# Performance work log

Measured on AMD Instinct MI355X. Metric: run time of the kernel, lower is better.

Reference implementation:

```python
import jax, jax.numpy as jnp
import numpy as np

B, S, D = 2, 2048, 1024
H = 16
HD = D // H
SCALE = float(np.sqrt(HD))


def setup_inputs() -> dict:
    key = jax.random.key(0)
    ks = jax.random.split(key, 10)
    def lin(k):
        # xavier_uniform for [out, in] = [D, D]
        bound = float(np.sqrt(6.0 / (D + D)))
        return jax.random.uniform(k, (D, D), jnp.float32, -bound, bound)
    return {
        "hidden_states": jax.random.normal(ks[0], (B, S, D), jnp.float32),
        "attention_mask": jnp.ones((B, S), jnp.float32),
        "Wq": lin(ks[1]), "bq": jnp.zeros((D,), jnp.float32),
        "Wk": lin(ks[2]), "bk": jnp.zeros((D,), jnp.float32),
        "Wv": lin(ks[3]), "bv": jnp.zeros((D,), jnp.float32),
        "Wo": lin(ks[4]), "bo": jnp.zeros((D,), jnp.float32),
    }


def _heads(x):
    # [B,S,D] -> [B,H,S,HD]
    return x.reshape(B, S, H, HD).transpose(0, 2, 1, 3)


def secure_softmax(scores):
    c = jnp.clip(scores, -3.0, 3.0)
    sig = 0.5 + 0.25 * c - 0.01 * c ** 3
    sig = jnp.clip(sig, 0.01, 0.99)
    return sig / (jnp.sum(sig, axis=-1, keepdims=True) + 1e-8)


def reference(hidden_states, attention_mask, Wq, bq, Wk, bk, Wv, bv, Wo, bo):
    q = _heads(hidden_states @ Wq.T + bq)
    k = _heads(hidden_states @ Wk.T + bk)
    v = _heads(hidden_states @ Wv.T + bv)
    # [B,H,S,S]
    scores = jnp.einsum("bhqd,bhkd->bhqk", q, k) / SCALE
    scores = scores + (1.0 - attention_mask[:, None, None, :]) * -10000.0
    probs = secure_softmax(scores)
    ctx = jnp.einsum("bhqk,bhkd->bhqd", probs, v)
    ctx = ctx.transpose(0, 2, 1, 3).reshape(B, S, D)
    return ctx @ Wo.T + bo
```

## Files before the change

### kernel.cpp

```cpp
#include <hip/hip_runtime.h>
#include <stdint.h>

#define B_ 2
#define S_ 2048
#define D_ 1024
#define H_ 16
#define HD_ 64
#define M_ (B_*S_)

typedef __bf16 bf16;
typedef __attribute__((ext_vector_type(8))) __bf16 bf16x8;
typedef __attribute__((ext_vector_type(4))) float f32x4;
typedef __attribute__((ext_vector_type(2))) float f32x2;

__device__ __forceinline__ void gload16(const bf16* g, bf16* l) {
    __builtin_amdgcn_global_load_lds(
        (const __attribute__((address_space(1))) void*)g,
        (__attribute__((address_space(3))) void*)l, 16, 0, 0);
}

__global__ void k_cvt_all(const float* __restrict__ hs,
                          const float* __restrict__ Wq, const float* __restrict__ Wk,
                          const float* __restrict__ Wv, const float* __restrict__ Wo,
                          bf16* __restrict__ hb,
                          bf16* __restrict__ wqb, bf16* __restrict__ wkb,
                          bf16* __restrict__ wvb, bf16* __restrict__ wob) {
    int blk = blockIdx.x;
    const float* s; bf16* d; int base;
    if (blk < 2048) { s = hs; d = hb; base = blk; }
    else {
        int r = blk - 2048; int which = r >> 9; base = r & 511;
        s = (which==0)?Wq:(which==1)?Wk:(which==2)?Wv:Wo;
        d = (which==0)?wqb:(which==1)?wkb:(which==2)?wvb:wob;
    }
    int idx = base*2048 + threadIdx.x*8;
    float4 a = *(const float4*)(s + idx);
    float4 b = *(const float4*)(s + idx + 4);
    bf16 o[8] = {(bf16)a.x,(bf16)a.y,(bf16)a.z,(bf16)a.w,
                 (bf16)b.x,(bf16)b.y,(bf16)b.z,(bf16)b.w};
    *(int4*)(d + idx) = *(const int4*)o;
}

__global__ __launch_bounds__(256) void k_gemm_qkv(
    const bf16* __restrict__ X,
    const bf16* __restrict__ Wq, const bf16* __restrict__ Wk, const bf16* __restrict__ Wv,
    const float* __restrict__ bq, const float* __restrict__ bk, const float* __restrict__ bv,
    bf16* __restrict__ Qo, bf16* __restrict__ Ko, bf16* __restrict__ Vo)
{
    const int z = blockIdx.z;
    const bf16* W = (z==0) ? Wq : (z==1) ? Wk : Wv;
    const float* bias = (z==0) ? bq : (z==1) ? bk : bv;
    const int n0 = blockIdx.x * 128;
    const int m0 = blockIdx.y * 128;
    const int t = threadIdx.x;
    const int w = t >> 6, lane = t & 63, quad = lane >> 4, l15 = lane & 15;
    const int lr = lane >> 3;
    const int lc = (lane & 7) ^ lr;
    const int sx = l15 & 7;
    const int mw = (w >> 1) * 64, nw = (w & 1) * 64;

    __shared__ __align__(16) char smraw[128*136*2];
    bf16* As  = (bf16*)smraw;
    bf16* Bs  = (bf16*)(smraw + 16384);
    bf16* epi = (bf16*)smraw;

    f32x4 acc[4][4];
    #pragma unroll
    for (int i = 0; i < 4; i++)
        #pragma unroll
        for (int j = 0; j < 4; j++)
            acc[i][j] = (f32x4){0.f,0.f,0.f,0.f};

    const bf16* gA = X + (size_t)(m0 + w*8 + lr)*D_ + lc*8;
    const bf16* gB = W + (size_t)(n0 + w*8 + lr)*D_ + lc*8;

    for (int k0 = 0; k0 < D_; k0 += 64) {
        #pragma unroll
        for (int c = 0; c < 4; c++) {
            gload16(gA + (size_t)c*32*D_ + k0, &As[c*2048 + w*512]);
            gload16(gB + (size_t)c*32*D_ + k0, &Bs[c*2048 + w*512]);
        }
        __syncthreads();
        #pragma unroll
        for (int ks = 0; ks < 2; ks++) {
            bf16x8 af[4], bfr[4];
            #pragma unroll
            for (int i = 0; i < 4; i++)
                af[i] = *(const bf16x8*)&As[(mw + i*16 + l15)*64 + (((ks*4+quad)^sx)*8)];
            #pragma unroll
            for (int j = 0; j < 4; j++)
                bfr[j] = *(const bf16x8*)&Bs[(nw + j*16 + l15)*64 + (((ks*4+quad)^sx)*8)];
            #pragma unroll
            for (int i = 0; i < 4; i++)
                #pragma unroll
                for (int j = 0; j < 4; j++)
                    acc[i][j] = __builtin_amdgcn_mfma_f32_16x16x32_bf16(af[i], bfr[j], acc[i][j], 0, 0, 0);
        }
        __syncthreads();
    }

    const float scale = (z == 0) ? 0.125f : 1.0f;
    if (z == 2) {
        #pragma unroll
        for (int j = 0; j < 4; j++) {
            int n = nw + j*16 + l15;
            float bn = bias[n0 + n];
            #pragma unroll
            for (int i = 0; i < 4; i++) {
                int mloc = mw + i*16 + quad*4;
                union { bf16 h4[4]; uint2 u; } pk;
                #pragma unroll
                for (int r = 0; r < 4; r++) pk.h4[r] = (bf16)(acc[i][j][r] + bn);
                *(uint2*)&epi[n*136 + mloc] = pk.u;
            }
        }
    } else {
        #pragma unroll
        for (int j = 0; j < 4; j++) {
            int n = nw + j*16 + l15;
            float bn = bias[n0 + n];
            #pragma unroll
            for (int i = 0; i < 4; i++) {
                int mloc = mw + i*16 + quad*4;
                #pragma unroll
                for (int r = 0; r < 4; r++)
                    epi[(mloc + r)*136 + n] = (bf16)((acc[i][j][r] + bn) * scale);
            }
        }
    }
    __syncthreads();
    if (z == 2) {
        #pragma unroll
        for (int kk = 0; kk < 8; kk++) {
            int c = t + 256*kk;
            int row = c >> 4;
            int mcol = (c & 15) * 8;
            int4 val = *(const int4*)&epi[row*136 + mcol];
            int n = n0 + row; int hh = n >> 6, hd = n & 63;
            int m = m0 + mcol; int bb = m >> 11, s = m & 2047;
            *(int4*)&Vo[((size_t)((bb*H_ + hh)*HD_ + hd))*S_ + s] = val;
        }
    } else {
        bf16* Out = (z == 0) ? Qo : Ko;
        #pragma unroll
        for (int kk = 0; kk < 8; kk++) {
            int c = t + 256*kk;
            int row = c >> 4;
            int ncol = (c & 15) * 8;
            int4 val = *(const int4*)&epi[row*136 + ncol];
            int m = m0 + row; int bb = m >> 11, s = m & 2047;
            int n = n0 + ncol; int hh = n >> 6, hd = n & 63;
            *(int4*)&Out[((size_t)((bb*H_ + hh)*S_ + s))*HD_ + hd] = val;
        }
    }
}

__global__ __launch_bounds__(256) void k_gemm_out(
    const bf16* __restrict__ X, const bf16* __restrict__ W,
    const float* __restrict__ bias, float* __restrict__ Out)
{
    const int n0 = blockIdx.x * 128;
    const int m0 = blockIdx.y * 64;
    const int t = threadIdx.x;
    const int w = t >> 6, lane = t & 63, quad = lane >> 4, l15 = lane & 15;
    const int lr = lane >> 3;
    const int lc = (lane & 7) ^ lr;
    const int sx = l15 & 7;
    const int nw = w * 32;

    __shared__ __align__(16) bf16 As[64*64];
    __shared__ __align__(16) bf16 Bs[128*64];

    f32x4 acc[4][2];
    #pragma unroll
    for (int i = 0; i < 4; i++)
        #pragma unroll
        for (int j = 0; j < 2; j++)
            acc[i][j] = (f32x4){0.f,0.f,0.f,0.f};

    const bf16* gA = X + (size_t)(m0 + w*8 + lr)*D_ + lc*8;
    const bf16* gB = W + (size_t)(n0 + w*8 + lr)*D_ + lc*8;

    for (int k0 = 0; k0 < D_; k0 += 64) {
        #pragma unroll
        for (int c = 0; c < 2; c++)
            gload16(gA + (size_t)c*32*D_ + k0, &As[c*2048 + w*512]);
        #pragma unroll
        for (int c = 0; c < 4; c++)
            gload16(gB + (size_t)c*32*D_ + k0, &Bs[c*2048 + w*512]);
        __syncthreads();
        #pragma unroll
        for (int ks = 0; ks < 2; ks++) {
            bf16x8 af[4], bfr[2];
            #pragma unroll
            for (int i = 0; i < 4; i++)
                af[i] = *(const bf16x8*)&As[(i*16 + l15)*64 + (((ks*4+quad)^sx)*8)];
            #pragma unroll
            for (int j = 0; j < 2; j++)
                bfr[j] = *(const bf16x8*)&Bs[(nw + j*16 + l15)*64 + (((ks*4+quad)^sx)*8)];
            #pragma unroll
            for (int i = 0; i < 4; i++)
                #pragma unroll
                for (int j = 0; j < 2; j++)
                    acc[i][j] = __builtin_amdgcn_mfma_f32_16x16x32_bf16(af[i], bfr[j], acc[i][j], 0, 0, 0);
        }
        __syncthreads();
    }

    #pragma unroll
    for (int j = 0; j < 2; j++) {
        int n = n0 + nw + j*16 + l15;
        float bn = bias[n];
        #pragma unroll
        for (int i = 0; i < 4; i++) {
            int mbase = m0 + i*16 + quad*4;
            #pragma unroll
            for (int r = 0; r < 4; r++)
                Out[(size_t)(mbase + r)*D_ + n] = acc[i][j][r] + bn;
        }
    }
}

__global__ __launch_bounds__(256, 2) void k_attn(
    const bf16* __restrict__ Q, const bf16* __restrict__ K, const bf16* __restrict__ Vt,
    const float* __restrict__ mask, bf16* __restrict__ Ctx)
{
    const int bh = blockIdx.y;
    const int b = bh >> 4, h = bh & 15;
    const int q0 = blockIdx.x * 128;
    const int t = threadIdx.x;
    const int w = t >> 6, lane = t & 63, quad = lane >> 4, l15 = lane & 15;
    const int lr = lane >> 3;
    const int lcV = (lane & 7) ^ lr;
    const int lcK = (lane & 7) ^ ((lr & 3) | ((w & 1) << 2));
    const int sx = l15 & 7;
    const int arow = ((l15 & 12) << 1) | (l15 & 3);

    __shared__ __align__(16) bf16 Ks[4][64*64];
    __shared__ __align__(16) bf16 Vs[4][64*64];
    __shared__ __align__(16) float Ms[S_];

    bf16x8 qf[2][2];
    const bf16* Qbase = Q + ((size_t)bh*S_ + q0 + w*32)*HD_;
    #pragma unroll
    for (int m2 = 0; m2 < 2; m2++)
        #pragma unroll
        for (int ks = 0; ks < 2; ks++)
            qf[m2][ks] = *(const bf16x8*)&Qbase[(size_t)(m2*16 + l15)*HD_ + ks*32 + quad*8];

    f32x4 cacc[2][4];
    #pragma unroll
    for (int i = 0; i < 2; i++)
        #pragma unroll
        for (int j = 0; j < 4; j++)
            cacc[i][j] = (f32x4){0.f,0.f,0.f,0.f};
    f32x2 lacv[2];
    #pragma unroll
    for (int m2 = 0; m2 < 2; m2++) lacv[m2] = (f32x2){0.f,0.f};

    const bf16* KstK = K  + ((size_t)bh*S_  + w*8 + lr)*HD_ + lcK*8;
    const bf16* VstV = Vt + ((size_t)bh*HD_ + w*8 + lr)*S_  + lcV*8;

    {
        const float* mg = mask + (size_t)b*S_ + t*8;
        float4 a0 = *(const float4*)mg;
        float4 a1 = *(const float4*)(mg + 4);
        *(float4*)&Ms[t*8]     = a0;
        *(float4*)&Ms[t*8 + 4] = a1;
    }
    #pragma unroll
    for (int pt = 0; pt < 2; pt++)
        #pragma unroll
        for (int c = 0; c < 2; c++) {
            gload16(KstK + (size_t)(pt*64 + c*32)*HD_, &Ks[pt][c*2048 + w*512]);
            gload16(VstV + (size_t)c*32*S_ + pt*64,    &Vs[pt][c*2048 + w*512]);
        }
    asm volatile("s_waitcnt vmcnt(4) lgkmcnt(0)\n\ts_barrier" ::: "memory");

    const int NT = S_/64;
    for (int it = 0; it < NT; it++) {
        const int cur = it & 3;
        const int k0 = it*64;

        if (it < NT-2) {
            const int pb = (it + 2) & 3;
            const int kp = k0 + 128;
            #pragma unroll
            for (int c = 0; c < 2; c++) {
                gload16(KstK + (size_t)(kp + c*32)*HD_, &Ks[pb][c*2048 + w*512]);
                gload16(VstV + (size_t)c*32*S_ + kp,    &Vs[pb][c*2048 + w*512]);
            }
        }

        f32x4 st[4][2];
        #pragma unroll
        for (int g = 0; g < 4; g++) {
            float4 m4 = *(const float4*)&Ms[k0 + quad*8 + (g>>1)*32 + (g&1)*4];
            f32x4 sti = (f32x4){m4.x, m4.y, m4.z, m4.w} * 10000.f - 10000.f;
            st[g][0] = sti;
            st[g][1] = sti;
        }

        __builtin_amdgcn_s_setprio(1);
        #pragma unroll
        for (int ks = 0; ks < 2; ks++) {
            #pragma unroll
            for (int g = 0; g < 4; g++) {
                const int kk = g >> 1, hf = g & 1;
                bf16x8 af = *(const bf16x8*)&Ks[cur][(arow + hf*4 + kk*32)*64 + (((ks*4+quad)^sx)*8)];
                #pragma unroll
                for (int m2 = 0; m2 < 2; m2++)
                    st[g][m2] = __builtin_amdgcn_mfma_f32_16x16x32_bf16(af, qf[m2][ks], st[g][m2], 0, 0, 0);
            }
        }
        __builtin_amdgcn_s_setprio(0);

        const f32x2 vn3 = {-3.f, -3.f}, vp3 = {3.f, 3.f};
        bf16x8 pa[2][2];
        #pragma unroll
        for (int m2 = 0; m2 < 2; m2++) {
            #pragma unroll
            for (int kk = 0; kk < 2; kk++) {
                union { bf16 h8[8]; bf16x8 v; } pk;
                #pragma unroll
                for (int hf = 0; hf < 2; hf++) {
                    f32x4 sv = st[kk*2 + hf][m2];
                    f32x2 lo = {sv[0], sv[1]};
                    f32x2 hi = {sv[2], sv[3]};
                    lo = __builtin_elementwise_min(__builtin_elementwise_max(lo, vn3), vp3);
                    hi = __builtin_elementwise_min(__builtin_elementwise_max(hi, vn3), vp3);
                    f32x2 tlo = lo * lo * (-0.01f) + 0.25f;
                    f32x2 thi = hi * hi * (-0.01f) + 0.25f;
                    f32x2 slo = lo * tlo + 0.5f;
                    f32x2 shi = hi * thi + 0.5f;
                    lacv[m2] += slo;
                    lacv[m2] += shi;
                    pk.h8[hf*4+0] = (bf16)slo.x; pk.h8[hf*4+1] = (bf16)slo.y;
                    pk.h8[hf*4+2] = (bf16)shi.x; pk.h8[hf*4+3] = (bf16)shi.y;
                }
                pa[m2][kk] = pk.v;
            }
        }

        #pragma unroll
        for (int kk = 0; kk < 2; kk++) {
            bf16x8 vf[4];
            #pragma unroll
            for (int nt = 0; nt < 4; nt++)
                vf[nt] = *(const bf16x8*)&Vs[cur][(nt*16 + l15)*64 + (((kk*4+quad)^sx)*8)];
            __builtin_amdgcn_s_setprio(1);
            #pragma unroll
            for (int m2 = 0; m2 < 2; m2++)
                #pragma unroll
                for (int nt = 0; nt < 4; nt++)
                    cacc[m2][nt] = __builtin_amdgcn_mfma_f32_16x16x32_bf16(pa[m2][kk], vf[nt], cacc[m2][nt], 0, 0, 0);
            __builtin_amdgcn_s_setprio(0);
        }

        if (it < NT-2)
            asm volatile("s_waitcnt vmcnt(4)\n\ts_barrier" ::: "memory");
        else
            asm volatile("s_waitcnt vmcnt(0)\n\ts_barrier" ::: "memory");
    }

    float s[2];
    #pragma unroll
    for (int m2 = 0; m2 < 2; m2++) {
        float v = lacv[m2].x + lacv[m2].y;
        v += __shfl_xor(v, 16);
        v += __shfl_xor(v, 32);
        s[m2] = v;
    }

    #pragma unroll
    for (int m2 = 0; m2 < 2; m2++) {
        #pragma unroll
        for (int r = 0; r < 4; r++) {
            float rs = __shfl(s[m2], quad*4 + r);
            float rinv = 1.0f / (rs + 1e-8f);
            size_t row = (size_t)(b*S_ + q0 + w*32 + m2*16 + quad*4 + r);
            #pragma unroll
            for (int nt = 0; nt < 4; nt++)
                Ctx[row*D_ + h*HD_ + nt*16 + l15] = (bf16)(cacc[m2][nt][r] * rinv);
        }
    }
}

extern "C" void kernel_launch(void* const* d_in, const int* in_sizes, int n_in,
                              void* d_out, int out_size, void* d_ws, size_t ws_size,
                              hipStream_t stream) {
    const float* hs   = (const float*)d_in[0];
    const float* mask = (const float*)d_in[1];
    const float* Wq   = (const float*)d_in[2];
    const float* bq   = (const float*)d_in[3];
    const float* Wk   = (const float*)d_in[4];
    const float* bk   = (const float*)d_in[5];
    const float* Wv   = (const float*)d_in[6];
    const float* bv   = (const float*)d_in[7];
    const float* Wo   = (const float*)d_in[8];
    const float* bo   = (const float*)d_in[9];
    float* out = (float*)d_out;

    char* ws = (char*)d_ws;
    const size_t MB = 1024*1024;
    bf16* hb   = (bf16*)(ws);
    bf16* wqb  = (bf16*)(ws + 8*MB);
    bf16* wkb  = (bf16*)(ws + 10*MB);
    bf16* wvb  = (bf16*)(ws + 12*MB);
    bf16* wob  = (bf16*)(ws + 14*MB);
    bf16* qb   = (bf16*)(ws + 16*MB);
    bf16* kb   = (bf16*)(ws + 24*MB);
    bf16* vtb  = (bf16*)(ws + 32*MB);
    bf16* ctxb = (bf16*)(ws + 40*MB);

    k_cvt_all<<<2048 + 4*512, 256, 0, stream>>>(hs, Wq, Wk, Wv, Wo, hb, wqb, wkb, wvb, wob);

    k_gemm_qkv<<<dim3(D_/128, M_/128, 3), 256, 0, stream>>>(
        hb, wqb, wkb, wvb, bq, bk, bv, qb, kb, vtb);

    k_attn<<<dim3(S_/128, B_*H_), 256, 0, stream>>>(qb, kb, vtb, mask, ctxb);

    k_gemm_out<<<dim3(D_/128, M_/64), 256, 0, stream>>>(ctxb, wob, bo, out);
}
```

Baseline: 200.9 us.

## Restructure attention K/V pipeline into paired 128-key stages with full waits

After: 195.5 us. 1.03x faster.

```diff
diff --git a/kernel.cpp b/kernel.cpp
--- a/kernel.cpp
+++ b/kernel.cpp
@@ -221,6 +221,92 @@
     }
 }
 
+#define ATT_PAIR(BUFA, K0, PF)                                                  \
+  {                                                                             \
+    if (PF) {                                                                   \
+      const int kp = (K0) + 128;                                                \
+      _Pragma("unroll")                                                         \
+      for (int c = 0; c < 2; c++) {                                             \
+        gload16(KstK + (size_t)(kp + c*32)*HD_,      &Ks[(BUFA)^2][c*2048 + w*512]);     \
+        gload16(VstV + (size_t)c*32*S_ + kp,         &Vs[(BUFA)^2][c*2048 + w*512]);     \
+        gload16(KstK + (size_t)(kp + 64 + c*32)*HD_, &Ks[((BUFA)^2)+1][c*2048 + w*512]); \
+        gload16(VstV + (size_t)c*32*S_ + kp + 64,    &Vs[((BUFA)^2)+1][c*2048 + w*512]); \
+      }                                                                         \
+    }                                                                           \
+    f32x4 st[2][4][2];                                                          \
+    _Pragma("unroll")                                                           \
+    for (int sub = 0; sub < 2; sub++) {                                         \
+      const int kb = (K0) + sub*64;                                             \
+      _Pragma("unroll")                                                         \
+      for (int g = 0; g < 4; g++) {                                             \
+        float4 m4 = *(const float4*)&Ms[kb + quad*8 + (g>>1)*32 + (g&1)*4];     \
+        f32x4 sti = (f32x4){m4.x, m4.y, m4.z, m4.w} * 10000.f - 10000.f;        \
+        st[sub][g][0] = sti;                                                    \
+        st[sub][g][1] = sti;                                                    \
+      }                                                                         \
+    }                                                                           \
+    __builtin_amdgcn_s_setprio(1);                                              \
+    _Pragma("unroll")                                                           \
+    for (int sub = 0; sub < 2; sub++) {                                         \
+      _Pragma("unroll")                                                         \
+      for (int ks = 0; ks < 2; ks++) {                                          \
+        _Pragma("unroll")                                                       \
+        for (int g = 0; g < 4; g++) {                                           \
+          const int kk = g >> 1, hf = g & 1;                                    \
+          bf16x8 af = *(const bf16x8*)&Ks[(BUFA)+sub][(arow + hf*4 + kk*32)*64 + (((ks*4+quad)^sx)*8)]; \
+          _Pragma("unroll")                                                     \
+          for (int m2 = 0; m2 < 2; m2++)                                        \
+            st[sub][g][m2] = __builtin_amdgcn_mfma_f32_16x16x32_bf16(af, qf[m2][ks], st[sub][g][m2], 0, 0, 0); \
+        }                                                                       \
+      }                                                                         \
+    }                                                                           \
+    __builtin_amdgcn_s_setprio(0);                                              \
+    _Pragma("unroll")                                                           \
+    for (int sub = 0; sub < 2; sub++) {                                         \
+      const f32x2 vn3 = {-3.f, -3.f}, vp3 = {3.f, 3.f};                         \
+      bf16x8 pa[2][2];                                                          \
+      _Pragma("unroll")                                                         \
+      for (int m2 = 0; m2 < 2; m2++) {                                          \
+        _Pragma("unroll")                                                       \
+        for (int kk = 0; kk < 2; kk++) {                                        \
+          union { bf16 h8[8]; bf16x8 v; } pk;                                   \
+          _Pragma("unroll")                                                     \
+          for (int hf = 0; hf < 2; hf++) {                                      \
+            f32x4 sv = st[sub][kk*2 + hf][m2];                                  \
+            f32x2 lo = {sv[0], sv[1]};                                          \
+            f32x2 hi = {sv[2], sv[3]};                                          \
+            lo = __builtin_elementwise_min(__builtin_elementwise_max(lo, vn3), vp3); \
+            hi = __builtin_elementwise_min(__builtin_elementwise_max(hi, vn3), vp3); \
+            f32x2 tlo = lo * lo * (-0.01f) + 0.25f;                             \
+            f32x2 thi = hi * hi * (-0.01f) + 0.25f;                             \
+            f32x2 slo = lo * tlo + 0.5f;                                        \
+            f32x2 shi = hi * thi + 0.5f;                                        \
+            lacv[m2] += slo;                                                    \
+            lacv[m2] += shi;                                                    \
+            pk.h8[hf*4+0] = (bf16)slo.x; pk.h8[hf*4+1] = (bf16)slo.y;           \
+            pk.h8[hf*4+2] = (bf16)shi.x; pk.h8[hf*4+3] = (bf16)shi.y;           \
+          }                                                                     \
+          pa[m2][kk] = pk.v;                                                    \
+        }                                                                       \
+      }                                                                         \
+      _Pragma("unroll")                                                         \
+      for (int kk = 0; kk < 2; kk++) {                                          \
+        bf16x8 vf[4];                                                           \
+        _Pragma("unroll")                                                       \
+        for (int nt = 0; nt < 4; nt++)                                          \
+          vf[nt] = *(const bf16x8*)&Vs[(BUFA)+sub][(nt*16 + l15)*64 + (((kk*4+quad)^sx)*8)]; \
+        __builtin_amdgcn_s_setprio(1);                                          \
+        _Pragma("unroll")                                                       \
+        for (int m2 = 0; m2 < 2; m2++)                                          \
+          _Pragma("unroll")                                                     \
+          for (int nt = 0; nt < 4; nt++)                                        \
+            cacc[m2][nt] = __builtin_amdgcn_mfma_f32_16x16x32_bf16(pa[m2][kk], vf[nt], cacc[m2][nt], 0, 0, 0); \
+        __builtin_amdgcn_s_setprio(0);                                          \
+      }                                                                         \
+    }                                                                           \
+    asm volatile("s_waitcnt vmcnt(0)\n\ts_barrier" ::: "memory");               \
+  }
+
 __global__ __launch_bounds__(256, 2) void k_attn(
     const bf16* __restrict__ Q, const bf16* __restrict__ K, const bf16* __restrict__ Vt,
     const float* __restrict__ mask, bf16* __restrict__ Ctx)
@@ -269,98 +355,18 @@
         *(float4*)&Ms[t*8 + 4] = a1;
     }
     #pragma unroll
-    for (int pt = 0; pt < 2; pt++)
-        #pragma unroll
-        for (int c = 0; c < 2; c++) {
-            gload16(KstK + (size_t)(pt*64 + c*32)*HD_, &Ks[pt][c*2048 + w*512]);
-            gload16(VstV + (size_t)c*32*S_ + pt*64,    &Vs[pt][c*2048 + w*512]);
-        }
-    asm volatile("s_waitcnt vmcnt(4) lgkmcnt(0)\n\ts_barrier" ::: "memory");
-
-    const int NT = S_/64;
-    for (int it = 0; it < NT; it++) {
-        const int cur = it & 3;
-        const int k0 = it*64;
-
-        if (it < NT-2) {
-            const int pb = (it + 2) & 3;
-            const int kp = k0 + 128;
-            #pragma unroll
-            for (int c = 0; c < 2; c++) {
-                gload16(KstK + (size_t)(kp + c*32)*HD_, &Ks[pb][c*2048 + w*512]);
-                gload16(VstV + (size_t)c*32*S_ + kp,    &Vs[pb][c*2048 + w*512]);
-            }
-        }
-
-        f32x4 st[4][2];
-        #pragma unroll
-        for (int g = 0; g < 4; g++) {
-            float4 m4 = *(const float4*)&Ms[k0 + quad*8 + (g>>1)*32 + (g&1)*4];
-            f32x4 sti = (f32x4){m4.x, m4.y, m4.z, m4.w} * 10000.f - 10000.f;
-            st[g][0] = sti;
-            st[g][1] = sti;
-        }
-
-        __builtin_amdgcn_s_setprio(1);
-        #pragma unroll
-        for (int ks = 0; ks < 2; ks++) {
-            #pragma unroll
-            for (int g = 0; g < 4; g++) {
-                const int kk = g >> 1, hf = g & 1;
-                bf16x8 af = *(const bf16x8*)&Ks[cur][(arow + hf*4 + kk*32)*64 + (((ks*4+quad)^sx)*8)];
-                #pragma unroll
-                for (int m2 = 0; m2 < 2; m2++)
-                    st[g][m2] = __builtin_amdgcn_mfma_f32_16x16x32_bf16(af, qf[m2][ks], st[g][m2], 0, 0, 0);
-            }
-        }
-        __builtin_amdgcn_s_setprio(0);
-
-        const f32x2 vn3 = {-3.f, -3.f}, vp3 = {3.f, 3.f};
-        bf16x8 pa[2][2];
-        #pragma unroll
-        for (int m2 = 0; m2 < 2; m2++) {
-            #pragma unroll
-            for (int kk = 0; kk < 2; kk++) {
-                union { bf16 h8[8]; bf16x8 v; } pk;
-                #pragma unroll
-                for (int hf = 0; hf < 2; hf++) {
-                    f32x4 sv = st[kk*2 + hf][m2];
-                    f32x2 lo = {sv[0], sv[1]};
-                    f32x2 hi = {sv[2], sv[3]};
-                    lo = __builtin_elementwise_min(__builtin_elementwise_max(lo, vn3), vp3);
-                    hi = __builtin_elementwise_min(__builtin_elementwise_max(hi, vn3), vp3);
-                    f32x2 tlo = lo * lo * (-0.01f) + 0.25f;
-                    f32x2 thi = hi * hi * (-0.01f) + 0.25f;
-                    f32x2 slo = lo * tlo + 0.5f;
-                    f32x2 shi = hi * thi + 0.5f;
-                    lacv[m2] += slo;
-                    lacv[m2] += shi;
-                    pk.h8[hf*4+0] = (bf16)slo.x; pk.h8[hf*4+1] = (bf16)slo.y;
-                    pk.h8[hf*4+2] = (bf16)shi.x; pk.h8[hf*4+3] = (bf16)shi.y;
-                }
-                pa[m2][kk] = pk.v;
-            }
-        }
-
-        #pragma unroll
-        for (int kk = 0; kk < 2; kk++) {
-            bf16x8 vf[4];
-            #pragma unroll
-            for (int nt = 0; nt < 4; nt++)
-                vf[nt] = *(const bf16x8*)&Vs[cur][(nt*16 + l15)*64 + (((kk*4+quad)^sx)*8)];
-            __builtin_amdgcn_s_setprio(1);
-            #pragma unroll
-            for (int m2 = 0; m2 < 2; m2++)
-                #pragma unroll
-                for (int nt = 0; nt < 4; nt++)
-                    cacc[m2][nt] = __builtin_amdgcn_mfma_f32_16x16x32_bf16(pa[m2][kk], vf[nt], cacc[m2][nt], 0, 0, 0);
-            __builtin_amdgcn_s_setprio(0);
-        }
-
-        if (it < NT-2)
-            asm volatile("s_waitcnt vmcnt(4)\n\ts_barrier" ::: "memory");
-        else
-            asm volatile("s_waitcnt vmcnt(0)\n\ts_barrier" ::: "memory");
+    for (int c = 0; c < 2; c++) {
+        gload16(KstK + (size_t)(c*32)*HD_,      &Ks[0][c*2048 + w*512]);
+        gload16(VstV + (size_t)c*32*S_,         &Vs[0][c*2048 + w*512]);
+        gload16(KstK + (size_t)(64 + c*32)*HD_, &Ks[1][c*2048 + w*512]);
+        gload16(VstV + (size_t)c*32*S_ + 64,    &Vs[1][c*2048 + w*512]);
+    }
+    asm volatile("s_waitcnt vmcnt(0) lgkmcnt(0)\n\ts_barrier" ::: "memory");
+
+    for (int q2 = 0; q2 < S_/256; q2++) {
+        const int k0 = q2 * 256;
+        ATT_PAIR(0, k0,        true);
+        ATT_PAIR(2, k0 + 128,  (q2 < S_/256 - 1));
     }
 
     float s[2];
```
